# Kernel optimization log

Measured on AMD Instinct MI355X. Metric: run time of the kernel, lower is better.

The kernel has to match this reference:

```python
import jax, jax.numpy as jnp
import numpy as np

DIM = 384
NUM_HEADS = 12
WIN = (8, 8, 8)
Q_TOK = 1
K_TOK = 1
B = 64
N = WIN[0] * WIN[1] * WIN[2]  # 512


def _build_rel_index():
    t = max(Q_TOK, K_TOK)
    max_rel = [(w - 1) * t for w in WIN]
    nbins = [2 * m + 1 for m in max_rel]
    def coords(tok):
        axes = [np.arange(WIN[i]) * tok for i in range(3)]
        g = np.stack(np.meshgrid(*axes, indexing='ij'))  # [3, D, H, W]
        return g.reshape(3, -1)  # [3, N]
    cq = coords(Q_TOK)
    ck = coords(K_TOK)
    rel = (cq[:, :, None] - ck[:, None, :]).transpose(1, 2, 0)  # [N, N, 3]
    rel = rel + np.array(max_rel)
    idx = rel[..., 0] * (nbins[1] * nbins[2]) + rel[..., 1] * nbins[2] + rel[..., 2]
    return idx.astype(np.int32), nbins[0] * nbins[1] * nbins[2]


def setup_inputs() -> dict:
    key = jax.random.key(0)
    ks = jax.random.split(key, 7)
    rel_index_np, num_rel = _build_rel_index()
    s = 0.02
    return {
        'x1': jax.random.normal(ks[0], (B, N, DIM), jnp.float32),
        'x2': jax.random.normal(ks[1], (B, N, DIM), jnp.float32),
        'Wq': jax.random.normal(ks[2], (DIM, DIM), jnp.float32) * s,
        'Wkv': jax.random.normal(ks[3], (2 * DIM, DIM), jnp.float32) * s,
        'q_bias': jax.random.normal(ks[4], (DIM,), jnp.float32) * s,
        'v_bias': jax.random.normal(ks[5], (DIM,), jnp.float32) * s,
        'bias_table': jax.random.normal(ks[6], (num_rel, NUM_HEADS), jnp.float32) * s,
        'rel_index': jnp.asarray(rel_index_np),  # [N, N] int32
    }


def reference(x1, x2, Wq, Wkv, q_bias, v_bias, bias_table, rel_index):
    Bq, N1, C = x1.shape
    N2 = x2.shape[1]
    H = NUM_HEADS
    hd = C // H

    q = x1 @ Wq.T + q_bias                      # [B, N1, C]
    kv_bias = jnp.concatenate([jnp.zeros_like(v_bias), v_bias])
    kv = x2 @ Wkv.T + kv_bias                   # [B, N2, 2C]

    q = q.reshape(Bq, N1, H, hd).transpose(0, 2, 1, 3)   # [B, H, N1, hd]
    kv = kv.reshape(Bq, N2, 2, H, hd).transpose(2, 0, 3, 1, 4)
    k, v = kv[0], kv[1]                          # [B, H, N2, hd]

    # relative position bias: gather [N1, N2, H] -> [H, N1, N2]
    bias = bias_table[rel_index]                 # [N1, N2, H]
    bias = bias.transpose(2, 0, 1)               # [H, N1, N2]

    scale = 1.0 / jnp.sqrt(jnp.asarray(hd, q.dtype))
    scores = jnp.einsum('bhqd,bhkd->bhqk', q, k) * scale + bias[None]
    attn = jax.nn.softmax(scores, axis=-1)
    out = jnp.einsum('bhqk,bhkd->bhqd', attn, v)  # [B, H, N1, hd]
    return out.transpose(0, 2, 1, 3).reshape(Bq, N1, C)
```

## Files before the change

kernel.cpp:

```cpp
#include <hip/hip_runtime.h>

typedef unsigned short u16;
typedef unsigned int u32;
typedef __bf16 bf16x8 __attribute__((ext_vector_type(8)));
typedef float f32x4 __attribute__((ext_vector_type(4)));
typedef float f32x16 __attribute__((ext_vector_type(16)));
typedef u16 u16x8 __attribute__((ext_vector_type(8)));
typedef u32 u32x4 __attribute__((ext_vector_type(4)));

#define NB 64
#define NN 512
#define NH 12
#define HD 32
#define DIM 384

static constexpr size_t QWS = (size_t)NB * NH * NN * HD;
#define LOG2E 1.4426950408889634f
#define QSCALE 0.25503486f

__device__ __forceinline__ u16 f2bf(float f) {
  __bf16 b = (__bf16)f;
  union { __bf16 b; u16 u; } v; v.b = b;
  return v.u;
}
__device__ __forceinline__ float lo16f(u32 w) {
  union { u32 u; float f; } v; v.u = w << 16;
  return v.f;
}
__device__ __forceinline__ float hi16f(u32 w) {
  union { u32 u; float f; } v; v.u = w & 0xffff0000u;
  return v.f;
}
__device__ __forceinline__ void gload16(const void* g, void* l) {
  __builtin_amdgcn_global_load_lds((const __attribute__((address_space(1))) u32*)g,
                                   (__attribute__((address_space(3))) u32*)l, 16, 0, 0);
}

__global__ __launch_bounds__(256) void prep_k(const float* __restrict__ table,
                                              const int* __restrict__ rel,
                                              const float* __restrict__ Wq,
                                              const float* __restrict__ Wkv,
                                              u32* __restrict__ beR,
                                              u16* __restrict__ Wf) {
  int bid = blockIdx.x;
  if (bid < 6144) {
    int t = bid * 256 + threadIdx.x;
    int word = t & 3;
    int lane = (t >> 2) & 63;
    int mf   = (t >> 8) & 3;
    int wv   = (t >> 10) & 7;
    int kt   = (t >> 13) & 15;
    int h    = t >> 17;
    int lr = lane & 15, lg = lane >> 4;
    int q = wv * 64 + mf * 16 + lr;
    int k = kt * 32 + (word >> 1) * 16 + lg * 4 + (word & 1) * 2;
    int i0 = rel[q * NN + k];
    int i1 = rel[q * NN + k + 1];
    u16 b0 = f2bf(table[i0 * NH + h] * LOG2E);
    u16 b1 = f2bf(table[i1 * NH + h] * LOG2E);
    beR[t] = (u32)b0 | ((u32)b1 << 16);
  } else {
    int t2 = (bid - 6144) * 256 + threadIdx.x;
    int lane = t2 & 63;
    int kk = (t2 >> 6) % 24;
    int cb = t2 / (24 * 64);
    int j = cb * 32 + (lane & 31);
    int k = kk * 16 + (lane >> 5) * 8;
    const float* wrow = (j < 384) ? (Wq + (size_t)j * DIM) : (Wkv + (size_t)(j - 384) * DIM);
    float4 a = *(const float4*)(wrow + k);
    float4 b = *(const float4*)(wrow + k + 4);
    u16x8 o = {f2bf(a.x), f2bf(a.y), f2bf(a.z), f2bf(a.w),
               f2bf(b.x), f2bf(b.y), f2bf(b.z), f2bf(b.w)};
    *(u16x8*)(Wf + (size_t)t2 * 8) = o;
  }
}

__global__ __launch_bounds__(256, 2) void qkv_proj_k(const float* __restrict__ x1,
                                                     const float* __restrict__ x2,
                                                     const float* __restrict__ qb,
                                                     const float* __restrict__ vb,
                                                     const u16* __restrict__ Wf,
                                                     u16* __restrict__ q_ws,
                                                     u16* __restrict__ k_ws,
                                                     u16* __restrict__ v_ws) {
  __shared__ __attribute__((aligned(16))) u16 Wbuf[2][12288];

  const int g = blockIdx.x;
  const int vv = (g & 7) * 96 + (g >> 3);
  const int type = vv >> 8;
  const int m0 = (vv & 255) * 128;
  const int tid = threadIdx.x, lane = tid & 63, w = tid >> 6;
  const int lo = lane & 31, hi = lane >> 5;
  const float* X = (type == 0) ? x1 : x2;
  const int bb = m0 >> 9, m0r = m0 & 511;
  const char* wsrc = (const char*)(Wf + (size_t)type * 12 * 12288);

  bf16x8 af[24];
  const float* xrow = X + (size_t)(m0 + w * 32 + lo) * DIM + hi * 8;
#pragma unroll
  for (int kk = 0; kk < 24; ++kk) {
    float4 a = *(const float4*)(xrow + kk * 16);
    float4 b = *(const float4*)(xrow + kk * 16 + 4);
    af[kk] = (bf16x8){(__bf16)a.x, (__bf16)a.y, (__bf16)a.z, (__bf16)a.w,
                      (__bf16)b.x, (__bf16)b.y, (__bf16)b.z, (__bf16)b.w};
  }

#pragma unroll
  for (int i = 0; i < 6; ++i) {
    int inst = w * 6 + i;
    gload16(wsrc + inst * 1024 + lane * 16, (char*)&Wbuf[0][0] + inst * 1024 + lane * 16);
  }
  __syncthreads();

  u16* dst = (type == 0) ? q_ws : (type == 1 ? k_ws : v_ws);
  const float scale = (type == 0) ? QSCALE : 1.0f;

  for (int c = 0; c < 12; ++c) {
    if (c + 1 < 12) {
      const char* s = wsrc + (size_t)(c + 1) * 24576;
      char* d = (char*)&Wbuf[(c + 1) & 1][0];
#pragma unroll
      for (int i = 0; i < 6; ++i) {
        int inst = w * 6 + i;
        gload16(s + inst * 1024 + lane * 16, d + inst * 1024 + lane * 16);
      }
    }
    const u16* wb = &Wbuf[c & 1][0];
    f32x16 acc = {};
#pragma unroll
    for (int kk = 0; kk < 24; ++kk) {
      bf16x8 wf = *(const bf16x8*)(wb + kk * 512 + lane * 8);
      acc = __builtin_amdgcn_mfma_f32_32x32x16_bf16(af[kk], wf, acc, 0, 0, 0);
    }
    float bv = (type == 0) ? qb[c * 32 + lo] : (type == 2 ? vb[c * 32 + lo] : 0.0f);
    u16* dbase = dst + (((size_t)(bb * NH + c) * NN) + m0r + w * 32) * HD + lo;
#pragma unroll
    for (int reg = 0; reg < 16; ++reg) {
      int row = (reg & 3) + 8 * (reg >> 2) + 4 * hi;
      dbase[(size_t)row * HD] = f2bf((acc[reg] + bv) * scale);
    }
    __syncthreads();
  }
}

__global__ __launch_bounds__(512, 4) void attn_k(const u16* __restrict__ qw,
                                                 const u16* __restrict__ kw,
                                                 const u16* __restrict__ vw,
                                                 const u32* __restrict__ beR,
                                                 float* __restrict__ out) {
  const int g = blockIdx.x;
  const int vv = (g & 7) * 96 + (g >> 3);
  const int h = vv >> 6, b = vv & 63;
  const size_t base = ((size_t)b * NH + h) * NN * HD;
  const u16* Q = qw + base;
  const u16* K = kw + base;
  const u16* V = vw + base;

  __shared__ u16 Ks[NN][40];
  __shared__ u16 Vtp[HD][520];

  const int tid = threadIdx.x;
  const int lane = tid & 63, w = tid >> 6;
  const int lg = lane >> 4, lr = lane & 15;
  const int q0 = w * 64;

  bf16x8 qf[4];
#pragma unroll
  for (int mf = 0; mf < 4; ++mf)
    qf[mf] = *(const bf16x8*)&Q[(q0 + mf * 16 + lr) * HD + lg * 8];

  for (int c = tid; c < 2048; c += 512) {
    int row = c >> 2, part = (c & 3) * 8;
    *(u16x8*)&Ks[row][part] = *(const u16x8*)&K[row * HD + part];
    u16x8 vld = *(const u16x8*)&V[row * HD + part];
    int kk = row & 31;
    int col = (row & ~31) + ((kk >> 2) & 3) * 8 + (kk >> 4) * 4 + (kk & 3);
#pragma unroll
    for (int j = 0; j < 8; ++j) Vtp[part + j][col] = vld[j];
  }
  __syncthreads();

  const u32* bstream = beR + ((((size_t)h * 16) * 8 + w) * 4) * 256 + lane * 4;

  f32x4 accOT[4][2] = {};
  float lsum[4] = {0.f, 0.f, 0.f, 0.f};

  for (int kt = 0; kt < 16; ++kt) {
    const int k0 = kt * 32;
    const u32* bkt = bstream + (size_t)kt * 8192;
    bf16x8 kf0 = *(const bf16x8*)&Ks[k0 + lr][lg * 8];
    bf16x8 kf1 = *(const bf16x8*)&Ks[k0 + 16 + lr][lg * 8];
    bf16x8 vp0 = *(const bf16x8*)&Vtp[lr][k0 + lg * 8];
    bf16x8 vp1 = *(const bf16x8*)&Vtp[16 + lr][k0 + lg * 8];
#pragma unroll
    for (int mf = 0; mf < 4; ++mf) {
      u32x4 bbv = *(const u32x4*)(bkt + mf * 256);
      f32x4 c0 = {lo16f(bbv.x), hi16f(bbv.x), lo16f(bbv.y), hi16f(bbv.y)};
      f32x4 c1 = {lo16f(bbv.z), hi16f(bbv.z), lo16f(bbv.w), hi16f(bbv.w)};
      f32x4 s0 = __builtin_amdgcn_mfma_f32_16x16x32_bf16(kf0, qf[mf], c0, 0, 0, 0);
      f32x4 s1 = __builtin_amdgcn_mfma_f32_16x16x32_bf16(kf1, qf[mf], c1, 0, 0, 0);
      float p0[4], p1[4];
#pragma unroll
      for (int r = 0; r < 4; ++r) {
        p0[r] = __builtin_amdgcn_exp2f(s0[r]);
        p1[r] = __builtin_amdgcn_exp2f(s1[r]);
      }
      lsum[mf] += ((p0[0] + p0[1]) + (p0[2] + p0[3])) +
                  ((p1[0] + p1[1]) + (p1[2] + p1[3]));
      bf16x8 pv = {(__bf16)p0[0], (__bf16)p0[1], (__bf16)p0[2], (__bf16)p0[3],
                   (__bf16)p1[0], (__bf16)p1[1], (__bf16)p1[2], (__bf16)p1[3]};
      accOT[mf][0] = __builtin_amdgcn_mfma_f32_16x16x32_bf16(vp0, pv, accOT[mf][0], 0, 0, 0);
      accOT[mf][1] = __builtin_amdgcn_mfma_f32_16x16x32_bf16(vp1, pv, accOT[mf][1], 0, 0, 0);
    }
  }

  float linv[4];
#pragma unroll
  for (int mf = 0; mf < 4; ++mf) {
    float s = lsum[mf];
    s += __shfl_xor(s, 16, 64);
    s += __shfl_xor(s, 32, 64);
    linv[mf] = 1.0f / s;
  }

  float* outp = out + ((size_t)b * NN) * DIM + h * HD;
#pragma unroll
  for (int mf = 0; mf < 4; ++mf) {
    int q = q0 + mf * 16 + lr;
#pragma unroll
    for (int nf = 0; nf < 2; ++nf) {
      float4 o = {accOT[mf][nf][0] * linv[mf], accOT[mf][nf][1] * linv[mf],
                  accOT[mf][nf][2] * linv[mf], accOT[mf][nf][3] * linv[mf]};
      *(float4*)&outp[(size_t)q * DIM + nf * 16 + lg * 4] = o;
    }
  }
}

extern "C" void kernel_launch(void* const* d_in, const int* in_sizes, int n_in,
                              void* d_out, int out_size, void* d_ws, size_t ws_size,
                              hipStream_t stream) {
  const float* x1    = (const float*)d_in[0];
  const float* x2    = (const float*)d_in[1];
  const float* Wq    = (const float*)d_in[2];
  const float* Wkv   = (const float*)d_in[3];
  const float* qb    = (const float*)d_in[4];
  const float* vb    = (const float*)d_in[5];
  const float* table = (const float*)d_in[6];
  const int*   rel   = (const int*)d_in[7];
  float* out = (float*)d_out;

  u16* ws   = (u16*)d_ws;
  u16* q_ws = ws;
  u16* k_ws = ws + QWS;
  u16* v_ws = ws + 2 * QWS;
  u32* beR  = (u32*)(ws + 3 * QWS);
  u16* Wf   = ws + 3 * QWS + 2 * 1572864;

  prep_k<<<6360, 256, 0, stream>>>(table, rel, Wq, Wkv, beR, Wf);
  qkv_proj_k<<<768, 256, 0, stream>>>(x1, x2, qb, vb, Wf, q_ws, k_ws, v_ws);
  attn_k<<<NB * NH, 512, 0, stream>>>(q_ws, k_ws, v_ws, beR, out);
}
```

Before: 113.6 us.

## Load projection weights directly from global memory instead of LDS double buffer

The QKV projection kernel no longer stages weight chunks through a double-buffered LDS array with global_load_lds and per-chunk barriers. Each wave now reads its weight fragments straight from global memory, which should hit in L2 since all blocks share the same weights. It also splits the 24-step MFMA chain into two independent accumulators to shorten the dependency chain, and adds asm barriers to keep the converted X fragments in registers. The risk is more global and L2 traffic per wave with no latency hiding beyond what the compiler schedules, in exchange for freeing LDS and removing the syncs.

```diff
diff --git a/kernel.cpp b/kernel.cpp
--- a/kernel.cpp
+++ b/kernel.cpp
@@ -30,10 +30,6 @@
 __device__ __forceinline__ float hi16f(u32 w) {
   union { u32 u; float f; } v; v.u = w & 0xffff0000u;
   return v.f;
-}
-__device__ __forceinline__ void gload16(const void* g, void* l) {
-  __builtin_amdgcn_global_load_lds((const __attribute__((address_space(1))) u32*)g,
-                                   (__attribute__((address_space(3))) u32*)l, 16, 0, 0);
 }
 
 __global__ __launch_bounds__(256) void prep_k(const float* __restrict__ table,
@@ -83,8 +79,6 @@
                                                      u16* __restrict__ q_ws,
                                                      u16* __restrict__ k_ws,
                                                      u16* __restrict__ v_ws) {
-  __shared__ __attribute__((aligned(16))) u16 Wbuf[2][12288];
-
   const int g = blockIdx.x;
   const int vv = (g & 7) * 96 + (g >> 3);
   const int type = vv >> 8;
@@ -93,7 +87,7 @@
   const int lo = lane & 31, hi = lane >> 5;
   const float* X = (type == 0) ? x1 : x2;
   const int bb = m0 >> 9, m0r = m0 & 511;
-  const char* wsrc = (const char*)(Wf + (size_t)type * 12 * 12288);
+  const u16* wsrc = Wf + (size_t)type * 147456 + lane * 8;
 
   bf16x8 af[24];
   const float* xrow = X + (size_t)(m0 + w * 32 + lo) * DIM + hi * 8;
@@ -104,42 +98,31 @@
     af[kk] = (bf16x8){(__bf16)a.x, (__bf16)a.y, (__bf16)a.z, (__bf16)a.w,
                       (__bf16)b.x, (__bf16)b.y, (__bf16)b.z, (__bf16)b.w};
   }
-
-#pragma unroll
-  for (int i = 0; i < 6; ++i) {
-    int inst = w * 6 + i;
-    gload16(wsrc + inst * 1024 + lane * 16, (char*)&Wbuf[0][0] + inst * 1024 + lane * 16);
-  }
-  __syncthreads();
+#pragma unroll
+  for (int kk = 0; kk < 24; ++kk)
+    asm volatile("" : "+v"(af[kk]));
 
   u16* dst = (type == 0) ? q_ws : (type == 1 ? k_ws : v_ws);
   const float scale = (type == 0) ? QSCALE : 1.0f;
 
   for (int c = 0; c < 12; ++c) {
-    if (c + 1 < 12) {
-      const char* s = wsrc + (size_t)(c + 1) * 24576;
-      char* d = (char*)&Wbuf[(c + 1) & 1][0];
-#pragma unroll
-      for (int i = 0; i < 6; ++i) {
-        int inst = w * 6 + i;
-        gload16(s + inst * 1024 + lane * 16, d + inst * 1024 + lane * 16);
-      }
-    }
-    const u16* wb = &Wbuf[c & 1][0];
-    f32x16 acc = {};
-#pragma unroll
-    for (int kk = 0; kk < 24; ++kk) {
-      bf16x8 wf = *(const bf16x8*)(wb + kk * 512 + lane * 8);
-      acc = __builtin_amdgcn_mfma_f32_32x32x16_bf16(af[kk], wf, acc, 0, 0, 0);
+    const u16* wc = wsrc + c * 12288;
+    f32x16 acc0 = {};
+    f32x16 acc1 = {};
+#pragma unroll
+    for (int kk = 0; kk < 12; ++kk) {
+      bf16x8 wfa = *(const bf16x8*)(wc + kk * 512);
+      bf16x8 wfb = *(const bf16x8*)(wc + (kk + 12) * 512);
+      acc0 = __builtin_amdgcn_mfma_f32_32x32x16_bf16(af[kk],      wfa, acc0, 0, 0, 0);
+      acc1 = __builtin_amdgcn_mfma_f32_32x32x16_bf16(af[kk + 12], wfb, acc1, 0, 0, 0);
     }
     float bv = (type == 0) ? qb[c * 32 + lo] : (type == 2 ? vb[c * 32 + lo] : 0.0f);
     u16* dbase = dst + (((size_t)(bb * NH + c) * NN) + m0r + w * 32) * HD + lo;
 #pragma unroll
     for (int reg = 0; reg < 16; ++reg) {
       int row = (reg & 3) + 8 * (reg >> 2) + 4 * hi;
-      dbase[(size_t)row * HD] = f2bf((acc[reg] + bv) * scale);
-    }
-    __syncthreads();
+      dbase[(size_t)row * HD] = f2bf((acc0[reg] + acc1[reg] + bv) * scale);
+    }
   }
 }
 
```

New measurement: 159.2 us. +40.1%, slower.
